# Kernel tuning notes

Measured on AMD Instinct MI355X. Metric: run time of the kernel, lower is better.

The kernel has to match this reference:

```python
import jax, jax.numpy as jnp
import numpy as np

N_NODES = 100000
N_EDGES = 1600000
D = 128          # h_size == feature_representation_size
N_CLASSES = 2
N_GRAPHS = 64


def setup_inputs() -> dict:
    key = jax.random.key(0)
    ks = jax.random.split(key, 8)
    scale = 1.0 / np.sqrt(D)
    x = jax.random.normal(ks[0], (N_NODES, D), jnp.float32)
    edge_index = jax.random.randint(ks[1], (2, N_EDGES), 0, N_NODES, dtype=jnp.int64)
    batch = jnp.sort(jax.random.randint(ks[2], (N_NODES,), 0, N_GRAPHS, dtype=jnp.int64))
    W0 = jax.random.normal(ks[3], (D, D), jnp.float32) * scale
    W1 = jax.random.normal(ks[4], (D, D), jnp.float32) * scale
    W2 = jax.random.normal(ks[5], (D, D), jnp.float32) * scale
    Wf = jax.random.normal(ks[6], (D, N_CLASSES), jnp.float32) * scale
    return dict(
        x=x, edge_index=edge_index, batch=batch,
        W0=W0, b0=jnp.zeros((D,), jnp.float32),
        W1=W1, b1=jnp.zeros((D,), jnp.float32),
        W2=W2, b2=jnp.zeros((D,), jnp.float32),
        Wf=Wf, bf=jnp.zeros((N_CLASSES,), jnp.float32),
    )


def gcn_norm(edge_index, num_nodes):
    # add self loops, symmetric normalization D^{-1/2} A_hat D^{-1/2}
    src, dst = edge_index[0], edge_index[1]
    loop = jnp.arange(num_nodes, dtype=src.dtype)
    src = jnp.concatenate([src, loop])
    dst = jnp.concatenate([dst, loop])
    ew = jnp.ones(src.shape[0], jnp.float32)
    deg = jax.ops.segment_sum(ew, dst, num_segments=num_nodes)
    dinv = jnp.where(deg > 0, jax.lax.rsqrt(deg), 0.0)
    norm = dinv[src] * dinv[dst]  # [E+N]
    return src, dst, norm


def gcn_conv(h, W, b, src, dst, norm, num_nodes):
    h = h @ W                                   # linear transform
    msg = h[src] * norm[:, None]                # gather + scale over edges
    out = jax.ops.segment_sum(msg, dst, num_segments=num_nodes)  # scatter-add
    return out + b


def reference(x, edge_index, batch, W0, b0, W1, b1, W2, b2, Wf, bf):
    n = x.shape[0]
    src, dst, norm = gcn_norm(edge_index, n)
    h = jax.nn.relu(gcn_conv(x, W0, b0, src, dst, norm, n))
    h = jax.nn.relu(gcn_conv(h, W1, b1, src, dst, norm, n))
    h = gcn_conv(h, W2, b2, src, dst, norm, n)  # last layer, no relu
    pooled = jax.ops.segment_max(h, batch, num_segments=N_GRAPHS)  # global max pool
    return pooled @ Wf + bf
```

## Files before the change

### kernel.cpp

```cpp
#include <hip/hip_runtime.h>
#include <hip/hip_bf16.h>
#include <hip/hip_fp16.h>
#include <float.h>

#define D 128
#define NGRAPHS 64
#define BKSHIFT 9
#define BKNODES 512
#define MAXBK 256
#define PCH 4096

typedef _Float16 h8 __attribute__((ext_vector_type(8)));
typedef float f4 __attribute__((ext_vector_type(4)));

__device__ __forceinline__ unsigned fkey(float f){
  unsigned u = __float_as_uint(f);
  return (u & 0x80000000u) ? ~u : (u | 0x80000000u);
}
__device__ __forceinline__ float funkey(unsigned k){
  unsigned u = (k & 0x80000000u) ? (k ^ 0x80000000u) : ~k;
  return __uint_as_float(u);
}

__global__ __launch_bounds__(256) void k_bhist_w(const int* __restrict__ dst,
    int* __restrict__ bcnt, int E, int npart,
    const float* __restrict__ W0, const float* __restrict__ W1,
    const float* __restrict__ W2, _Float16* __restrict__ Wsw){
  if ((int)blockIdx.x >= npart){
    int layer = blockIdx.x - npart;
    const float* W = (layer == 0) ? W0 : (layer == 1) ? W1 : W2;
    _Float16* dstp = Wsw + (size_t)layer * 16384;
    int lane = threadIdx.x & 63;
    int quad = lane >> 4;
    int n    = lane & 15;
    for (int pair = (threadIdx.x >> 6); pair < 32; pair += 4){
      int k0 = pair >> 3;
      int tt = pair & 7;
      _Float16 v[8];
      #pragma unroll
      for (int j = 0; j < 8; j++){
        int k = k0 * 32 + quad * 8 + j;
        v[j] = (_Float16)W[k * 128 + 16 * tt + n];
      }
      *(uint4*)&dstp[((size_t)pair * 64 + lane) * 8] = *(uint4*)v;
    }
    return;
  }
  __shared__ int h[MAXBK];
  int t = threadIdx.x;
  for (int i = t; i < MAXBK; i += 256) h[i] = 0;
  __syncthreads();
  int e0 = blockIdx.x * PCH;
  #pragma unroll
  for (int j = 0; j < PCH / 256; j++){
    int e = e0 + t + j * 256;
    if (e < E) atomicAdd(&h[dst[e] >> BKSHIFT], 1);
  }
  __syncthreads();
  for (int i = t; i < MAXBK; i += 256) if (h[i]) atomicAdd(&bcnt[i], h[i]);
}

__global__ __launch_bounds__(256) void k_bscan(const int* __restrict__ bcnt,
    int* __restrict__ bOff, int* __restrict__ bCur, int* __restrict__ row_ptr,
    unsigned* __restrict__ pk, int nbk, int N, int E){
  __shared__ int sh[256];
  int t = threadIdx.x;
  for (int i = t; i < NGRAPHS * D; i += 256) pk[i] = 0u;
  int v = (t < nbk) ? bcnt[t] : 0;
  sh[t] = v; __syncthreads();
  for (int off = 1; off < 256; off <<= 1){
    int x = (t >= off) ? sh[t - off] : 0;
    __syncthreads();
    sh[t] += x;
    __syncthreads();
  }
  if (t < nbk){ int ex = sh[t] - v; bOff[t] = ex; bCur[t] = ex; }
  if (t == 0){ bOff[nbk] = E; row_ptr[N] = E; }
}

__global__ __launch_bounds__(256) void k_part(const int* __restrict__ src,
    const int* __restrict__ dst, int* __restrict__ bCur,
    uint2* __restrict__ epart, int E){
  __shared__ int scnt[MAXBK], soff[MAXBK], sbase[MAXBK], scur[MAXBK];
  __shared__ int stmp[256];
  __shared__ uint2 stage[PCH];
  int t = threadIdx.x;
  int e0 = blockIdx.x * PCH;
  int eN = E - e0; if (eN > PCH) eN = PCH;
  for (int i = t; i < MAXBK; i += 256){ scnt[i] = 0; scur[i] = 0; }
  __syncthreads();
  uint2 mye[PCH / 256];
  #pragma unroll
  for (int j = 0; j < PCH / 256; j++){
    int e = e0 + t + j * 256;
    if (e < E){
      mye[j].x = (unsigned)src[e];
      mye[j].y = (unsigned)dst[e];
      atomicAdd(&scnt[mye[j].y >> BKSHIFT], 1);
    }
  }
  __syncthreads();
  int v = scnt[t];
  stmp[t] = v; __syncthreads();
  for (int off = 1; off < 256; off <<= 1){
    int x = (t >= off) ? stmp[t - off] : 0;
    __syncthreads();
    stmp[t] += x;
    __syncthreads();
  }
  soff[t] = stmp[t] - v;
  if (v > 0) sbase[t] = atomicAdd(&bCur[t], v);
  __syncthreads();
  #pragma unroll
  for (int j = 0; j < PCH / 256; j++){
    int e = e0 + t + j * 256;
    if (e < E){
      int b = mye[j].y >> BKSHIFT;
      int l = atomicAdd(&scur[b], 1);
      stage[soff[b] + l] = mye[j];
    }
  }
  __syncthreads();
  for (int j = t; j < eN; j += 256){
    uint2 ed = stage[j];
    int b = (int)(ed.y >> BKSHIFT);
    epart[(size_t)sbase[b] + (j - soff[b])] = ed;
  }
}

__global__ __launch_bounds__(256) void k_bfill(const uint2* __restrict__ epart,
    const int* __restrict__ bOff, int* __restrict__ row_ptr,
    int* __restrict__ col, float* __restrict__ dinv, int N){
  __shared__ int hc[BKNODES], off[BKNODES], cur[BKNODES];
  __shared__ int stmp[256];
  int b = blockIdx.x, t = threadIdx.x;
  int base = bOff[b], cntE = bOff[b + 1] - base;
  int node0 = b << BKSHIFT;
  int nloc = N - node0; if (nloc > BKNODES) nloc = BKNODES;
  for (int i = t; i < BKNODES; i += 256) hc[i] = 0;
  __syncthreads();
  for (int j = t; j < cntE; j += 256){
    uint2 ed = epart[(size_t)base + j];
    atomicAdd(&hc[ed.y - node0], 1);
  }
  __syncthreads();
  int a0 = hc[2 * t], a1 = hc[2 * t + 1];
  int s = a0 + a1;
  stmp[t] = s; __syncthreads();
  for (int o = 1; o < 256; o <<= 1){
    int x = (t >= o) ? stmp[t - o] : 0;
    __syncthreads();
    stmp[t] += x;
    __syncthreads();
  }
  int ex = stmp[t] - s;
  off[2 * t] = ex; off[2 * t + 1] = ex + a0;
  __syncthreads();
  for (int i = t; i < nloc; i += 256){
    row_ptr[node0 + i] = base + off[i];
    dinv[node0 + i]    = rsqrtf((float)hc[i] + 1.0f);
    cur[i] = off[i];
  }
  __syncthreads();
  for (int j = t; j < cntE; j += 256){
    uint2 ed = epart[(size_t)base + j];
    int p = atomicAdd(&cur[ed.y - node0], 1);
    col[base + p] = (int)ed.x;
  }
}

__global__ __launch_bounds__(256) void gemm_mfma(const _Float16* __restrict__ A,
    const _Float16* __restrict__ Wsw, _Float16* __restrict__ C, int M){
  __shared__ _Float16 lds[4][16][136];
  int wave = threadIdx.x >> 6;
  int lane = threadIdx.x & 63;
  int quad = lane >> 4;
  int l15  = lane & 15;
  int m0 = blockIdx.x * 64 + wave * 16;
  if (m0 >= M) return;
  f4 acc[8] = {};
  h8 af[4];
  const _Float16* arow = A + (size_t)(m0 + l15) * D;
  #pragma unroll
  for (int k0 = 0; k0 < 4; k0++)
    af[k0] = *(const h8*)&arow[k0 * 32 + quad * 8];
  #pragma unroll
  for (int k0 = 0; k0 < 4; k0++){
    #pragma unroll
    for (int t = 0; t < 8; t++){
      h8 bf = *(const h8*)&Wsw[((size_t)(k0 * 8 + t) * 64 + lane) * 8];
      acc[t] = __builtin_amdgcn_mfma_f32_16x16x32_f16(af[k0], bf, acc[t], 0, 0, 0);
    }
  }
  #pragma unroll
  for (int t = 0; t < 8; t++){
    #pragma unroll
    for (int r = 0; r < 4; r++)
      lds[wave][quad * 4 + r][t * 16 + l15] = (_Float16)acc[t][r];
  }
  #pragma unroll
  for (int it = 0; it < 4; it++){
    int idx = it * 64 + lane;
    int row = idx >> 4;
    int ch  = idx & 15;
    *(uint4*)&C[(size_t)(m0 + row) * D + ch * 8] = *(uint4*)&lds[wave][row][ch * 8];
  }
}

__global__ __launch_bounds__(256) void gemm_mfma_f32A(const float* __restrict__ A,
    const _Float16* __restrict__ Wsw, _Float16* __restrict__ C, int M){
  __shared__ _Float16 lds[4][16][136];
  int wave = threadIdx.x >> 6;
  int lane = threadIdx.x & 63;
  int quad = lane >> 4;
  int l15  = lane & 15;
  int m0 = blockIdx.x * 64 + wave * 16;
  if (m0 >= M) return;
  f4 acc[8] = {};
  h8 af[4];
  const float* arow = A + (size_t)(m0 + l15) * D;
  #pragma unroll
  for (int k0 = 0; k0 < 4; k0++){
    float4 a = *(const float4*)&arow[k0 * 32 + quad * 8];
    float4 b = *(const float4*)&arow[k0 * 32 + quad * 8 + 4];
    __half2 p0 = __floats2half2_rn(a.x, a.y);
    __half2 p1 = __floats2half2_rn(a.z, a.w);
    __half2 p2 = __floats2half2_rn(b.x, b.y);
    __half2 p3 = __floats2half2_rn(b.z, b.w);
    union { uint4 u; h8 v; } cv;
    cv.u.x = *(unsigned*)&p0; cv.u.y = *(unsigned*)&p1;
    cv.u.z = *(unsigned*)&p2; cv.u.w = *(unsigned*)&p3;
    af[k0] = cv.v;
  }
  #pragma unroll
  for (int k0 = 0; k0 < 4; k0++){
    #pragma unroll
    for (int t = 0; t < 8; t++){
      h8 bf = *(const h8*)&Wsw[((size_t)(k0 * 8 + t) * 64 + lane) * 8];
      acc[t] = __builtin_amdgcn_mfma_f32_16x16x32_f16(af[k0], bf, acc[t], 0, 0, 0);
    }
  }
  #pragma unroll
  for (int t = 0; t < 8; t++){
    #pragma unroll
    for (int r = 0; r < 4; r++)
      lds[wave][quad * 4 + r][t * 16 + l15] = (_Float16)acc[t][r];
  }
  #pragma unroll
  for (int it = 0; it < 4; it++){
    int idx = it * 64 + lane;
    int row = idx >> 4;
    int ch  = idx & 15;
    *(uint4*)&C[(size_t)(m0 + row) * D + ch * 8] = *(uint4*)&lds[wave][row][ch * 8];
  }
}

__device__ __forceinline__ void accm(float* acc, uint4 u, float w){
  union { uint4 u; _Float16 h[8]; } cv;
  cv.u = u;
  #pragma unroll
  for (int k = 0; k < 8; k++)
    acc[k] += (float)cv.h[k] * w;
}

__global__ __launch_bounds__(256) void k_agg(const __half* __restrict__ t,
    const int* __restrict__ row_ptr, const int* __restrict__ col,
    const float* __restrict__ dinv, const float* __restrict__ bias,
    __half* __restrict__ outh, int relu, int N){
  int node = blockIdx.x * 4 + (threadIdx.x >> 6);
  if (node >= N) return;
  int lane = threadIdx.x & 63;
  int way  = lane >> 4;
  int cg   = (lane & 15) * 8;
  float di = dinv[node];
  int beg = row_ptr[node], end = row_ptr[node + 1];
  float acc[8] = {0.f,0.f,0.f,0.f,0.f,0.f,0.f,0.f};
  int j = beg + way;
  for (; j + 12 < end; j += 16){
    int s0 = col[j], s1 = col[j + 4], s2 = col[j + 8], s3 = col[j + 12];
    float w0 = dinv[s0] * di;
    float w1 = dinv[s1] * di;
    float w2 = dinv[s2] * di;
    float w3 = dinv[s3] * di;
    uint4 u0 = *(const uint4*)&t[(size_t)s0 * D + cg];
    uint4 u1 = *(const uint4*)&t[(size_t)s1 * D + cg];
    uint4 u2 = *(const uint4*)&t[(size_t)s2 * D + cg];
    uint4 u3 = *(const uint4*)&t[(size_t)s3 * D + cg];
    accm(acc, u0, w0);
    accm(acc, u1, w1);
    accm(acc, u2, w2);
    accm(acc, u3, w3);
  }
  for (; j < end; j += 4){
    int s = col[j];
    float w = dinv[s] * di;
    uint4 u = *(const uint4*)&t[(size_t)s * D + cg];
    accm(acc, u, w);
  }
  #pragma unroll
  for (int k = 0; k < 8; k++){
    acc[k] += __shfl_xor(acc[k], 16, 64);
    acc[k] += __shfl_xor(acc[k], 32, 64);
  }
  if (way == 0){
    uint4 su = *(const uint4*)&t[(size_t)node * D + cg];
    union { uint4 u; _Float16 h[8]; } sv; sv.u = su;
    float dii = di * di;
    float4 b0 = *(const float4*)&bias[cg];
    float4 b1 = *(const float4*)&bias[cg + 4];
    float bb[8] = {b0.x, b0.y, b0.z, b0.w, b1.x, b1.y, b1.z, b1.w};
    float o[8];
    #pragma unroll
    for (int k = 0; k < 8; k++)
      o[k] = acc[k] + (float)sv.h[k] * dii + bb[k];
    if (relu){
      #pragma unroll
      for (int k = 0; k < 8; k++) o[k] = fmaxf(o[k], 0.f);
    }
    __half2 p0 = __floats2half2_rn(o[0], o[1]);
    __half2 p1 = __floats2half2_rn(o[2], o[3]);
    __half2 p2 = __floats2half2_rn(o[4], o[5]);
    __half2 p3 = __floats2half2_rn(o[6], o[7]);
    uint4 u;
    u.x = *(unsigned*)&p0; u.y = *(unsigned*)&p1;
    u.z = *(unsigned*)&p2; u.w = *(unsigned*)&p3;
    *(uint4*)&outh[(size_t)node * D + cg] = u;
  }
}

__global__ __launch_bounds__(128) void k_pool(const __half* __restrict__ h,
    const int* __restrict__ batch, unsigned* __restrict__ pk, int N){
  int d = threadIdx.x;
  int n0 = blockIdx.x * 64;
  int nEnd = n0 + 64; if (nEnd > N) nEnd = N;
  float cur = -FLT_MAX;
  int curg = batch[n0];
  int n = n0;
  for (; n + 3 < nEnd; n += 4){
    const __half* r = &h[(size_t)n * D + d];
    __half v0 = r[0], v1 = r[D], v2 = r[2 * D], v3 = r[3 * D];
    int g0 = batch[n], g1 = batch[n + 1], g2 = batch[n + 2], g3 = batch[n + 3];
    if (g0 != curg){ atomicMax(&pk[curg * D + d], fkey(cur)); cur = -FLT_MAX; curg = g0; }
    cur = fmaxf(cur, __half2float(v0));
    if (g1 != curg){ atomicMax(&pk[curg * D + d], fkey(cur)); cur = -FLT_MAX; curg = g1; }
    cur = fmaxf(cur, __half2float(v1));
    if (g2 != curg){ atomicMax(&pk[curg * D + d], fkey(cur)); cur = -FLT_MAX; curg = g2; }
    cur = fmaxf(cur, __half2float(v2));
    if (g3 != curg){ atomicMax(&pk[curg * D + d], fkey(cur)); cur = -FLT_MAX; curg = g3; }
    cur = fmaxf(cur, __half2float(v3));
  }
  for (; n < nEnd; n++){
    int g = batch[n];
    if (g != curg){ atomicMax(&pk[curg * D + d], fkey(cur)); cur = -FLT_MAX; curg = g; }
    cur = fmaxf(cur, __half2float(h[(size_t)n * D + d]));
  }
  atomicMax(&pk[curg * D + d], fkey(cur));
}

__global__ __launch_bounds__(128) void k_final(const unsigned* __restrict__ pk,
    const float* __restrict__ Wf, const float* __restrict__ bf,
    float* __restrict__ out){
  int t = threadIdx.x;
  int g = t >> 1, c = t & 1;
  float s = bf[c];
  for (int k = 0; k < D; k++)
    s += funkey(pk[g * D + k]) * Wf[k * 2 + c];
  out[g * 2 + c] = s;
}

extern "C" void kernel_launch(void* const* d_in, const int* in_sizes, int n_in,
                              void* d_out, int out_size, void* d_ws, size_t ws_size,
                              hipStream_t stream){
  const float* x   = (const float*)d_in[0];
  const int*   ei  = (const int*)d_in[1];
  const int*   bat = (const int*)d_in[2];
  const float* W0  = (const float*)d_in[3];
  const float* b0  = (const float*)d_in[4];
  const float* W1  = (const float*)d_in[5];
  const float* b1  = (const float*)d_in[6];
  const float* W2  = (const float*)d_in[7];
  const float* b2  = (const float*)d_in[8];
  const float* Wf  = (const float*)d_in[9];
  const float* bf  = (const float*)d_in[10];
  int N = in_sizes[0] / D;
  int E = in_sizes[1] / 2;
  const int* srcp = ei;
  const int* dstp = ei + E;
  int nbk   = (N + BKNODES - 1) / BKNODES;
  int npart = (E + PCH - 1) / PCH;

  char* p = (char*)d_ws;
  auto alloc = [&](size_t bytes)->char*{
    char* r = p; p += (bytes + 255) & ~(size_t)255; return r;
  };
  float*     dinv    = (float*)alloc((size_t)N * 4);
  int*       row_ptr = (int*)alloc((size_t)(N + 1) * 4);
  int*       col     = (int*)alloc((size_t)E * 4);
  uint2*     epart   = (uint2*)alloc((size_t)E * 8);
  _Float16*  tmp     = (_Float16*)alloc((size_t)N * D * 2);
  _Float16*  h16     = (_Float16*)alloc((size_t)N * D * 2);
  _Float16*  Wsw     = (_Float16*)alloc((size_t)3 * 16384 * 2);
  unsigned*  pk      = (unsigned*)alloc((size_t)NGRAPHS * D * 4);
  int*       bcnt    = (int*)alloc((size_t)MAXBK * 4);
  int*       bOff    = (int*)alloc((size_t)(MAXBK + 1) * 4);
  int*       bCur    = (int*)alloc((size_t)MAXBK * 4);

  hipMemsetAsync(bcnt, 0, (size_t)MAXBK * 4, stream);

  k_bhist_w<<<npart + 3, 256, 0, stream>>>(dstp, bcnt, E, npart, W0, W1, W2, Wsw);
  k_bscan<<<1, 256, 0, stream>>>(bcnt, bOff, bCur, row_ptr, pk, nbk, N, E);
  k_part<<<npart, 256, 0, stream>>>(srcp, dstp, bCur, epart, E);
  k_bfill<<<nbk, 256, 0, stream>>>(epart, bOff, row_ptr, col, dinv, N);

  int gblocks = (N + 63) / 64;
  int ablocks = (N + 3) / 4;
  gemm_mfma_f32A<<<gblocks, 256, 0, stream>>>(x, Wsw, tmp, N);
  k_agg<<<ablocks, 256, 0, stream>>>((const __half*)tmp, row_ptr, col, dinv, b0, (__half*)h16, 1, N);
  gemm_mfma<<<gblocks, 256, 0, stream>>>(h16, Wsw + 16384, tmp, N);
  k_agg<<<ablocks, 256, 0, stream>>>((const __half*)tmp, row_ptr, col, dinv, b1, (__half*)h16, 1, N);
  gemm_mfma<<<gblocks, 256, 0, stream>>>(h16, Wsw + 32768, tmp, N);
  k_agg<<<ablocks, 256, 0, stream>>>((const __half*)tmp, row_ptr, col, dinv, b2, (__half*)h16, 0, N);
  k_pool<<<(N + 63) / 64, 128, 0, stream>>>((const __half*)h16, bat, pk, N);
  k_final<<<1, 128, 0, stream>>>(pk, Wf, bf, (float*)d_out);
}
```

Before: 412.5 us.

## Fuse first-layer GEMM with degree histogram and weight conversion in one launch

Only W0 is now converted in a tiny first kernel, which also zeroes the bucket counters in place of the memset. A combined kernel then runs the layer-0 GEMM on x, the destination-bucket histogram and the W1/W2 conversion as separate block ranges, so the independent GEMM overlaps with graph preprocessing and launches are saved. The partition chunk size is halved to give k_part more blocks. The risk is heterogeneous blocks in one grid and larger LDS per histogram block, which could lower occupancy.

```diff
diff --git a/kernel.cpp b/kernel.cpp
--- a/kernel.cpp
+++ b/kernel.cpp
@@ -8,7 +8,7 @@
 #define BKSHIFT 9
 #define BKNODES 512
 #define MAXBK 256
-#define PCH 4096
+#define PCH 2048
 
 typedef _Float16 h8 __attribute__((ext_vector_type(8)));
 typedef float f4 __attribute__((ext_vector_type(4)));
@@ -22,42 +22,107 @@
   return __uint_as_float(u);
 }
 
-__global__ __launch_bounds__(256) void k_bhist_w(const int* __restrict__ dst,
-    int* __restrict__ bcnt, int E, int npart,
-    const float* __restrict__ W0, const float* __restrict__ W1,
-    const float* __restrict__ W2, _Float16* __restrict__ Wsw){
-  if ((int)blockIdx.x >= npart){
-    int layer = blockIdx.x - npart;
-    const float* W = (layer == 0) ? W0 : (layer == 1) ? W1 : W2;
-    _Float16* dstp = Wsw + (size_t)layer * 16384;
+__device__ __forceinline__ void wcvt_pair(const float* __restrict__ W,
+    _Float16* __restrict__ dstp, int pair, int lane){
+  int quad = lane >> 4;
+  int n    = lane & 15;
+  int k0 = pair >> 3;
+  int tt = pair & 7;
+  _Float16 v[8];
+  #pragma unroll
+  for (int j = 0; j < 8; j++){
+    int k = k0 * 32 + quad * 8 + j;
+    v[j] = (_Float16)W[k * 128 + 16 * tt + n];
+  }
+  *(uint4*)&dstp[((size_t)pair * 64 + lane) * 8] = *(uint4*)v;
+}
+
+__global__ __launch_bounds__(256) void k_wcvt0(const float* __restrict__ W0,
+    _Float16* __restrict__ Wsw, int* __restrict__ bcnt){
+  if (blockIdx.x == 0 && threadIdx.x < MAXBK) bcnt[threadIdx.x] = 0;
+  int lane = threadIdx.x & 63;
+  int pair = blockIdx.x * 4 + (threadIdx.x >> 6);
+  wcvt_pair(W0, Wsw, pair, lane);
+}
+
+#define HCH 4096
+__global__ __launch_bounds__(256) void k_mega(
+    const float* __restrict__ x, const _Float16* __restrict__ Wsw0,
+    _Float16* __restrict__ C, int M, int gb,
+    const int* __restrict__ dst, int* __restrict__ bcnt, int E, int nh,
+    const float* __restrict__ W1, const float* __restrict__ W2,
+    _Float16* __restrict__ Wsw12){
+  __shared__ __align__(16) char smraw[4 * 16 * 136 * 2];
+  int bid = blockIdx.x;
+  if (bid < gb){
+    _Float16 (*lds)[136] = (_Float16(*)[136])(smraw + (threadIdx.x >> 6) * 16 * 136 * 2);
     int lane = threadIdx.x & 63;
     int quad = lane >> 4;
-    int n    = lane & 15;
-    for (int pair = (threadIdx.x >> 6); pair < 32; pair += 4){
-      int k0 = pair >> 3;
-      int tt = pair & 7;
-      _Float16 v[8];
+    int l15  = lane & 15;
+    int m0 = bid * 64 + (threadIdx.x >> 6) * 16;
+    if (m0 >= M) return;
+    f4 acc[8] = {};
+    h8 af[4];
+    const float* arow = x + (size_t)(m0 + l15) * D;
+    #pragma unroll
+    for (int k0 = 0; k0 < 4; k0++){
+      float4 a = *(const float4*)&arow[k0 * 32 + quad * 8];
+      float4 b = *(const float4*)&arow[k0 * 32 + quad * 8 + 4];
+      __half2 p0 = __floats2half2_rn(a.x, a.y);
+      __half2 p1 = __floats2half2_rn(a.z, a.w);
+      __half2 p2 = __floats2half2_rn(b.x, b.y);
+      __half2 p3 = __floats2half2_rn(b.z, b.w);
+      union { uint4 u; h8 v; } cv;
+      cv.u.x = *(unsigned*)&p0; cv.u.y = *(unsigned*)&p1;
+      cv.u.z = *(unsigned*)&p2; cv.u.w = *(unsigned*)&p3;
+      af[k0] = cv.v;
+    }
+    #pragma unroll
+    for (int k0 = 0; k0 < 4; k0++){
       #pragma unroll
-      for (int j = 0; j < 8; j++){
-        int k = k0 * 32 + quad * 8 + j;
-        v[j] = (_Float16)W[k * 128 + 16 * tt + n];
+      for (int t = 0; t < 8; t++){
+        h8 bf = *(const h8*)&Wsw0[((size_t)(k0 * 8 + t) * 64 + lane) * 8];
+        acc[t] = __builtin_amdgcn_mfma_f32_16x16x32_f16(af[k0], bf, acc[t], 0, 0, 0);
       }
-      *(uint4*)&dstp[((size_t)pair * 64 + lane) * 8] = *(uint4*)v;
+    }
+    #pragma unroll
+    for (int t = 0; t < 8; t++){
+      #pragma unroll
+      for (int r = 0; r < 4; r++)
+        lds[quad * 4 + r][t * 16 + l15] = (_Float16)acc[t][r];
+    }
+    #pragma unroll
+    for (int it = 0; it < 4; it++){
+      int idx = it * 64 + lane;
+      int row = idx >> 4;
+      int ch  = idx & 15;
+      *(uint4*)&C[(size_t)(m0 + row) * D + ch * 8] = *(uint4*)&lds[row][ch * 8];
     }
     return;
   }
-  __shared__ int h[MAXBK];
-  int t = threadIdx.x;
-  for (int i = t; i < MAXBK; i += 256) h[i] = 0;
-  __syncthreads();
-  int e0 = blockIdx.x * PCH;
-  #pragma unroll
-  for (int j = 0; j < PCH / 256; j++){
-    int e = e0 + t + j * 256;
-    if (e < E) atomicAdd(&h[dst[e] >> BKSHIFT], 1);
-  }
-  __syncthreads();
-  for (int i = t; i < MAXBK; i += 256) if (h[i]) atomicAdd(&bcnt[i], h[i]);
+  bid -= gb;
+  if (bid < nh){
+    int* h = (int*)smraw;
+    int t = threadIdx.x;
+    for (int i = t; i < MAXBK; i += 256) h[i] = 0;
+    __syncthreads();
+    int e0 = bid * HCH;
+    #pragma unroll
+    for (int j = 0; j < HCH / 256; j++){
+      int e = e0 + t + j * 256;
+      if (e < E) atomicAdd(&h[dst[e] >> BKSHIFT], 1);
+    }
+    __syncthreads();
+    for (int i = t; i < MAXBK; i += 256) if (h[i]) atomicAdd(&bcnt[i], h[i]);
+    return;
+  }
+  bid -= nh;
+  const float* W = (bid < 2) ? W1 : W2;
+  _Float16* dstp = Wsw12 + ((bid < 2) ? 0 : 16384);
+  int pbase = (bid & 1) * 16;
+  int lane = threadIdx.x & 63;
+  for (int pp = (threadIdx.x >> 6); pp < 16; pp += 4)
+    wcvt_pair(W, dstp, pbase + pp, lane);
 }
 
 __global__ __launch_bounds__(256) void k_bscan(const int* __restrict__ bcnt,
@@ -184,54 +249,6 @@
   #pragma unroll
   for (int k0 = 0; k0 < 4; k0++)
     af[k0] = *(const h8*)&arow[k0 * 32 + quad * 8];
-  #pragma unroll
-  for (int k0 = 0; k0 < 4; k0++){
-    #pragma unroll
-    for (int t = 0; t < 8; t++){
-      h8 bf = *(const h8*)&Wsw[((size_t)(k0 * 8 + t) * 64 + lane) * 8];
-      acc[t] = __builtin_amdgcn_mfma_f32_16x16x32_f16(af[k0], bf, acc[t], 0, 0, 0);
-    }
-  }
-  #pragma unroll
-  for (int t = 0; t < 8; t++){
-    #pragma unroll
-    for (int r = 0; r < 4; r++)
-      lds[wave][quad * 4 + r][t * 16 + l15] = (_Float16)acc[t][r];
-  }
-  #pragma unroll
-  for (int it = 0; it < 4; it++){
-    int idx = it * 64 + lane;
-    int row = idx >> 4;
-    int ch  = idx & 15;
-    *(uint4*)&C[(size_t)(m0 + row) * D + ch * 8] = *(uint4*)&lds[wave][row][ch * 8];
-  }
-}
-
-__global__ __launch_bounds__(256) void gemm_mfma_f32A(const float* __restrict__ A,
-    const _Float16* __restrict__ Wsw, _Float16* __restrict__ C, int M){
-  __shared__ _Float16 lds[4][16][136];
-  int wave = threadIdx.x >> 6;
-  int lane = threadIdx.x & 63;
-  int quad = lane >> 4;
-  int l15  = lane & 15;
-  int m0 = blockIdx.x * 64 + wave * 16;
-  if (m0 >= M) return;
-  f4 acc[8] = {};
-  h8 af[4];
-  const float* arow = A + (size_t)(m0 + l15) * D;
-  #pragma unroll
-  for (int k0 = 0; k0 < 4; k0++){
-    float4 a = *(const float4*)&arow[k0 * 32 + quad * 8];
-    float4 b = *(const float4*)&arow[k0 * 32 + quad * 8 + 4];
-    __half2 p0 = __floats2half2_rn(a.x, a.y);
-    __half2 p1 = __floats2half2_rn(a.z, a.w);
-    __half2 p2 = __floats2half2_rn(b.x, b.y);
-    __half2 p3 = __floats2half2_rn(b.z, b.w);
-    union { uint4 u; h8 v; } cv;
-    cv.u.x = *(unsigned*)&p0; cv.u.y = *(unsigned*)&p1;
-    cv.u.z = *(unsigned*)&p2; cv.u.w = *(unsigned*)&p3;
-    af[k0] = cv.v;
-  }
   #pragma unroll
   for (int k0 = 0; k0 < 4; k0++){
     #pragma unroll
@@ -388,6 +405,8 @@
   const int* dstp = ei + E;
   int nbk   = (N + BKNODES - 1) / BKNODES;
   int npart = (E + PCH - 1) / PCH;
+  int nh    = (E + HCH - 1) / HCH;
+  int gb    = (N + 63) / 64;
 
   char* p = (char*)d_ws;
   auto alloc = [&](size_t bytes)->char*{
@@ -398,28 +417,26 @@
   int*       col     = (int*)alloc((size_t)E * 4);
   uint2*     epart   = (uint2*)alloc((size_t)E * 8);
   _Float16*  tmp     = (_Float16*)alloc((size_t)N * D * 2);
-  _Float16*  h16     = (_Float16*)alloc((size_t)N * D * 2);
+  _Float16*  tmp2    = (_Float16*)alloc((size_t)N * D * 2);
   _Float16*  Wsw     = (_Float16*)alloc((size_t)3 * 16384 * 2);
   unsigned*  pk      = (unsigned*)alloc((size_t)NGRAPHS * D * 4);
   int*       bcnt    = (int*)alloc((size_t)MAXBK * 4);
   int*       bOff    = (int*)alloc((size_t)(MAXBK + 1) * 4);
   int*       bCur    = (int*)alloc((size_t)MAXBK * 4);
 
-  hipMemsetAsync(bcnt, 0, (size_t)MAXBK * 4, stream);
-
-  k_bhist_w<<<npart + 3, 256, 0, stream>>>(dstp, bcnt, E, npart, W0, W1, W2, Wsw);
+  k_wcvt0<<<8, 256, 0, stream>>>(W0, Wsw, bcnt);
+  k_mega<<<gb + nh + 4, 256, 0, stream>>>(x, Wsw, tmp, N, gb,
+      dstp, bcnt, E, nh, W1, W2, Wsw + 16384);
   k_bscan<<<1, 256, 0, stream>>>(bcnt, bOff, bCur, row_ptr, pk, nbk, N, E);
   k_part<<<npart, 256, 0, stream>>>(srcp, dstp, bCur, epart, E);
   k_bfill<<<nbk, 256, 0, stream>>>(epart, bOff, row_ptr, col, dinv, N);
 
-  int gblocks = (N + 63) / 64;
   int ablocks = (N + 3) / 4;
-  gemm_mfma_f32A<<<gblocks, 256, 0, stream>>>(x, Wsw, tmp, N);
-  k_agg<<<ablocks, 256, 0, stream>>>((const __half*)tmp, row_ptr, col, dinv, b0, (__half*)h16, 1, N);
-  gemm_mfma<<<gblocks, 256, 0, stream>>>(h16, Wsw + 16384, tmp, N);
-  k_agg<<<ablocks, 256, 0, stream>>>((const __half*)tmp, row_ptr, col, dinv, b1, (__half*)h16, 1, N);
-  gemm_mfma<<<gblocks, 256, 0, stream>>>(h16, Wsw + 32768, tmp, N);
-  k_agg<<<ablocks, 256, 0, stream>>>((const __half*)tmp, row_ptr, col, dinv, b2, (__half*)h16, 0, N);
-  k_pool<<<(N + 63) / 64, 128, 0, stream>>>((const __half*)h16, bat, pk, N);
+  k_agg<<<ablocks, 256, 0, stream>>>((const __half*)tmp, row_ptr, col, dinv, b0, (__half*)tmp2, 1, N);
+  gemm_mfma<<<gb, 256, 0, stream>>>(tmp2, Wsw + 16384, tmp, N);
+  k_agg<<<ablocks, 256, 0, stream>>>((const __half*)tmp, row_ptr, col, dinv, b1, (__half*)tmp2, 1, N);
+  gemm_mfma<<<gb, 256, 0, stream>>>(tmp2, Wsw + 32768, tmp, N);
+  k_agg<<<ablocks, 256, 0, stream>>>((const __half*)tmp, row_ptr, col, dinv, b2, (__half*)tmp2, 0, N);
+  k_pool<<<(N + 63) / 64, 128, 0, stream>>>((const __half*)tmp2, bat, pk, N);
   k_final<<<1, 128, 0, stream>>>(pk, Wf, bf, (float*)d_out);
 }
```

After: 408.8 us. About the same (-0.9%).
